# Performance work log

Measured on AMD Instinct MI355X. Metric: run time of the kernel, lower is better.

The kernel has to match this reference:

```python
import jax, jax.numpy as jnp
import numpy as np

N = 50000
E = 800000
IN_FEAT = 256
HIDDEN = 256
NUM_CLASS = 10
NUM_GRAPHS = 512
LAYERS = 2


def setup_inputs() -> dict:
    key = jax.random.key(0)
    ks = jax.random.split(key, 10)
    x = jax.random.normal(ks[0], (N, IN_FEAT), dtype=jnp.float32)
    edge_index = jax.random.randint(ks[1], (2, E), 0, N, dtype=jnp.int32)
    batch = jnp.sort(jax.random.randint(ks[2], (N,), 0, NUM_GRAPHS, dtype=jnp.int32))
    s_in = 1.0 / np.sqrt(IN_FEAT)
    s_h = 1.0 / np.sqrt(HIDDEN)
    enc_W = jax.random.uniform(ks[3], (IN_FEAT, HIDDEN), jnp.float32, -s_in, s_in)
    enc_b = jax.random.uniform(ks[4], (HIDDEN,), jnp.float32, -s_in, s_in)
    conv_W = jax.random.uniform(ks[5], (LAYERS, HIDDEN, HIDDEN), jnp.float32, -s_h, s_h)
    conv_b = jax.random.uniform(ks[6], (LAYERS, HIDDEN), jnp.float32, -s_h, s_h)
    out_W = jax.random.uniform(ks[7], (HIDDEN, NUM_CLASS), jnp.float32, -s_h, s_h)
    out_b = jax.random.uniform(ks[8], (NUM_CLASS,), jnp.float32, -s_h, s_h)
    return {"x": x, "edge_index": edge_index, "batch": batch,
            "enc_W": enc_W, "enc_b": enc_b,
            "conv_W": conv_W, "conv_b": conv_b,
            "out_W": out_W, "out_b": out_b}


def _gcn_conv(x, row, col, deg_norm_edge, W, b):
    # PyG GCNConv: linear transform, then normalized scatter-add aggregation.
    h = x @ W                                   # [N, H]
    msg = h[row] * deg_norm_edge[:, None]       # [E+N, H] gather + scale
    out = jax.ops.segment_sum(msg, col, num_segments=N)  # scatter-add
    return out + b


def reference(x, edge_index, batch, enc_W, enc_b, conv_W, conv_b, out_W, out_b):
    # self-loops appended once (same structure every layer)
    loops = jnp.arange(N, dtype=edge_index.dtype)
    row = jnp.concatenate([edge_index[0], loops])  # source
    col = jnp.concatenate([edge_index[1], loops])  # target
    deg = jax.ops.segment_sum(jnp.ones_like(col, dtype=x.dtype), col, num_segments=N)
    dinv = jnp.where(deg > 0, jax.lax.rsqrt(deg), 0.0)
    norm = dinv[row] * dinv[col]                # symmetric GCN normalization per edge

    h = x @ enc_W + enc_b
    for i in range(LAYERS):
        h = jax.nn.relu(_gcn_conv(h, row, col, norm, conv_W[i], conv_b[i]))

    # global_mean_pool over `batch` segment ids
    sums = jax.ops.segment_sum(h, batch, num_segments=NUM_GRAPHS)
    cnts = jax.ops.segment_sum(jnp.ones((N,), dtype=h.dtype), batch, num_segments=NUM_GRAPHS)
    pooled = sums / jnp.maximum(cnts, 1.0)[:, None]

    # dropout is identity in eval mode
    return pooled @ out_W + out_b
```

## Files before the change

### kernel.cpp

```cpp
#include <hip/hip_runtime.h>

#define NN 50000
#define NE 800000
#define HD 256
#define NG 512
#define NC 10
#define TILES ((NN + 31) / 32)
#define GEMM_G 521
#define NP 196
#define HB 200
#define CHUNK (NE / HB)
#define NODES_PER_HB (NN / HB)

typedef unsigned short u16;
typedef unsigned char u8;
typedef short v8s __attribute__((ext_vector_type(8)));
typedef float v4f __attribute__((ext_vector_type(4)));
typedef float v2f __attribute__((ext_vector_type(2)));
typedef u16 v4u __attribute__((ext_vector_type(4)));
typedef u16 v8u __attribute__((ext_vector_type(8)));

static __device__ __forceinline__ float bf2f(u16 u) {
    return __uint_as_float(((unsigned)u) << 16);
}
static __device__ __forceinline__ u16 f2bf(float f) {
    unsigned u = __float_as_uint(f);
    unsigned r = (u + 0x7fffu + ((u >> 16) & 1u)) >> 16;
    return (u16)r;
}
static __device__ __forceinline__ int clampi(int v, int lo, int hi) {
    return min(max(v, lo), hi);
}
static __device__ __forceinline__ float ldf(const void* p, size_t i, int isbf) {
    return isbf ? bf2f(((const u16*)p)[i]) : ((const float*)p)[i];
}

static __device__ __forceinline__ u8 f32_to_fp8(float f) {
#if __has_builtin(__builtin_amdgcn_cvt_pk_fp8_f32)
    int r = __builtin_amdgcn_cvt_pk_fp8_f32(f, f, 0, false);
    return (u8)(r & 0xff);
#else
    float a = fabsf(f);
    unsigned s = (__float_as_uint(f) >> 31) << 7;
    if (a < 0.0009765625f) return (u8)s;
    a = fminf(a, 448.f);
    if (a < 0.015625f) {
        int m = (int)(a * 512.f + 0.5f);
        return (u8)(s | min(m, 7));
    }
    unsigned u = __float_as_uint(a);
    unsigned r = u + 0x0007FFFFu + ((u >> 20) & 1u);
    int e = (int)(r >> 23) - 127 + 7;
    if (e > 15) return (u8)(s | 0x7E);
    unsigned m = (r >> 20) & 7u;
    return (u8)(s | ((unsigned)e << 3) | m);
#endif
}
static __device__ __forceinline__ v4f fp8x4_to_f32(unsigned v) {
#if __has_builtin(__builtin_amdgcn_cvt_pk_f32_fp8)
    v2f lo = __builtin_amdgcn_cvt_pk_f32_fp8(v, false);
    v2f hi = __builtin_amdgcn_cvt_pk_f32_fp8(v, true);
    return (v4f){lo[0], lo[1], hi[0], hi[1]};
#else
    v4f o;
#pragma unroll
    for (int j = 0; j < 4; j++) {
        unsigned b = (v >> (8 * j)) & 0xffu;
        unsigned e = (b >> 3) & 15u, m = b & 7u;
        float val = e ? __uint_as_float(((e + 120u) << 23) | (m << 20))
                      : (float)m * 0.001953125f;
        o[j] = (b & 0x80u) ? -val : val;
    }
    return o;
#endif
}

__global__ void k_detect(const u16* __restrict__ xu, int* __restrict__ mode) {
    __shared__ int cnt;
    if (threadIdx.x == 0) cnt = 0;
    __syncthreads();
    int bad = 0;
    for (int i = threadIdx.x; i < 4096; i += 256) {
        float v = bf2f(xu[2 * i]);
        float av = fabsf(v);
        if (av > 100.f || (av < 1e-3f && av != 0.f)) bad++;
    }
    atomicAdd(&cnt, bad);
    __syncthreads();
    if (threadIdx.x == 0) mode[0] = (cnt > 1024) ? 0 : 1;
}

__global__ void k_prep(const void* __restrict__ enc_W, const void* __restrict__ conv_W,
                       const void* __restrict__ enc_b, const void* __restrict__ conv_b,
                       const void* __restrict__ out_b,
                       u16* __restrict__ Wp, float* __restrict__ biasf,
                       const int* __restrict__ modep) {
    int md = modep[0];
    int b = blockIdx.x;
    if (b < 768) {
        int wi = b >> 8;
        int n = b & 255, k = threadIdx.x;
        const void* W = (wi == 0) ? enc_W : conv_W;
        size_t off = (wi == 0) ? 0 : (size_t)(wi - 1) * HD * HD;
        int nt = n >> 4, m = n & 15;
        int ks = k >> 5, q = (k >> 3) & 3, j = k & 7;
        size_t idx = ((((size_t)nt * 8 + ks) * 64) + q * 16 + m) * 8 + j;
        Wp[(size_t)wi * HD * HD + idx] = f2bf(ldf(W, off + (size_t)k * HD + n, md));
    } else {
        for (int j = threadIdx.x; j < 768 + NC; j += 256) {
            float v = (j < 256) ? ldf(enc_b, j, md)
                    : (j < 768) ? ldf(conv_b, j - 256, md)
                                : ldf(out_b, j - 768, md);
            biasf[j] = v;
        }
    }
}

static __device__ __forceinline__ void hist_body(
        int b, int nthreads, const int* __restrict__ ecol,
        const int* __restrict__ batch,
        int* __restrict__ bh, int* __restrict__ gptr, int* hist) {
    int tid = threadIdx.x;
    if (tid < NP) hist[tid] = 0;
    __syncthreads();
    int e0 = b * CHUNK;
    for (int i = tid; i < CHUNK; i += nthreads) {
        int c = clampi(ecol[e0 + i], 0, NN - 1);
        atomicAdd(&hist[c >> 8], 1);
    }
    int n0 = b * NODES_PER_HB;
    for (int i = tid; i < NODES_PER_HB; i += nthreads) {
        int idx = n0 + i;
        int bb = clampi(batch[idx], 0, NG - 1);
        int bp = (idx == 0) ? -1 : clampi(batch[idx - 1], 0, NG - 1);
        for (int g = bp + 1; g <= bb; g++) gptr[g] = idx;
        if (idx == NN - 1)
            for (int g = bb + 1; g <= NG; g++) gptr[g] = NN;
    }
    __syncthreads();
    if (tid < NP) bh[(size_t)tid * HB + b] = hist[tid];
}

static __device__ __forceinline__ void scat_body(
        int b, int nthreads, const int* __restrict__ erow,
        const int* __restrict__ ecol,
        const int* __restrict__ pptr, const int* __restrict__ base,
        unsigned* __restrict__ pairbuf, int* lfill) {
    int tid = threadIdx.x;
    if (tid < NP) lfill[tid] = 0;
    __syncthreads();
    int e0 = b * CHUNK;
    for (int i = tid; i < CHUNK; i += nthreads) {
        int c = clampi(ecol[e0 + i], 0, NN - 1);
        int rw = clampi(erow[e0 + i], 0, NN - 1);
        int p = c >> 8;
        int r = atomicAdd(&lfill[p], 1);
        int pos = pptr[p] + base[(size_t)p * HB + b] + r;
        pairbuf[pos] = ((unsigned)rw << 8) | (unsigned)(c & 255);
    }
}

static __device__ __forceinline__ void gemm_body8(
        int gb, u16* As, const void* __restrict__ A, const u16* __restrict__ Wp,
        const float* __restrict__ biasf, void* __restrict__ out,
        int M, int hasBias, int outFp8, int amode) {
    int tid = threadIdx.x;
    int wave = tid >> 6;
    int lane = tid & 63;
    int m = lane & 15, q = lane >> 4;

    v8s bf[2][8];
#pragma unroll
    for (int nt = 0; nt < 2; nt++)
#pragma unroll
        for (int ks = 0; ks < 8; ks++)
            bf[nt][ks] = *(const v8s*)(Wp +
                ((size_t)((wave * 2 + nt) * 8 + ks) * 64 + lane) * 8);

    for (int tile = gb; tile < TILES; tile += GEMM_G) {
        int row0 = tile * 32;
#pragma unroll
        for (int it = 0; it < 2; it++) {
            int fb = it * 8 + wave;
            int mt = fb >> 3, ks = fb & 7;
            int row = min(row0 + mt * 16 + m, M - 1);
            int colE = ks * 32 + q * 8;
            v8s v;
            if (amode) {
                v = *(const v8s*)((const u16*)A + (size_t)row * HD + colE);
            } else {
                const float* af = (const float*)A + (size_t)row * HD + colE;
                v4f x0 = *(const v4f*)af;
                v4f x1 = *(const v4f*)(af + 4);
                v[0] = (short)f2bf(x0[0]); v[1] = (short)f2bf(x0[1]);
                v[2] = (short)f2bf(x0[2]); v[3] = (short)f2bf(x0[3]);
                v[4] = (short)f2bf(x1[0]); v[5] = (short)f2bf(x1[1]);
                v[6] = (short)f2bf(x1[2]); v[7] = (short)f2bf(x1[3]);
            }
            *(v8s*)&As[((size_t)fb * 64 + lane) * 8] = v;
        }
        __syncthreads();

        v4f acc[2][2];
#pragma unroll
        for (int i = 0; i < 2; i++)
#pragma unroll
            for (int j = 0; j < 2; j++) acc[i][j] = (v4f){0.f, 0.f, 0.f, 0.f};

#pragma unroll
        for (int ks = 0; ks < 8; ks++) {
            v8s a0 = *(const v8s*)&As[((size_t)ks * 64 + lane) * 8];
            v8s a1 = *(const v8s*)&As[((size_t)(8 + ks) * 64 + lane) * 8];
            acc[0][0] = __builtin_amdgcn_mfma_f32_16x16x32_bf16(
                a0, bf[0][ks], acc[0][0], 0, 0, 0);
            acc[0][1] = __builtin_amdgcn_mfma_f32_16x16x32_bf16(
                a0, bf[1][ks], acc[0][1], 0, 0, 0);
            acc[1][0] = __builtin_amdgcn_mfma_f32_16x16x32_bf16(
                a1, bf[0][ks], acc[1][0], 0, 0, 0);
            acc[1][1] = __builtin_amdgcn_mfma_f32_16x16x32_bf16(
                a1, bf[1][ks], acc[1][1], 0, 0, 0);
        }
        if (outFp8) {
#pragma unroll
            for (int mt = 0; mt < 2; mt++) {
#pragma unroll
                for (int nt = 0; nt < 2; nt++) {
                    int ocol = wave * 32 + nt * 16 + m;
#pragma unroll
                    for (int r = 0; r < 4; r++) {
                        int orow = row0 + mt * 16 + q * 4 + r;
                        if (orow < M)
                            ((u8*)out)[(size_t)orow * HD + ocol] =
                                f32_to_fp8(acc[mt][nt][r] * 32.f);
                    }
                }
            }
        } else {
#pragma unroll
            for (int mt = 0; mt < 2; mt++) {
#pragma unroll
                for (int nt = 0; nt < 2; nt++) {
                    int ocol = wave * 32 + nt * 16 + m;
                    float badd = hasBias ? biasf[ocol] : 0.f;
#pragma unroll
                    for (int r = 0; r < 4; r++) {
                        int orow = row0 + mt * 16 + q * 4 + r;
                        if (orow < M)
                            ((u16*)out)[(size_t)orow * HD + ocol] =
                                f2bf(acc[mt][nt][r] + badd);
                    }
                }
            }
        }
        __syncthreads();
    }
}

static __device__ __forceinline__ void agg_node(
        const u8* __restrict__ t, const int* __restrict__ cptr,
        const int* __restrict__ csrc, const float* __restrict__ dinv,
        const float* __restrict__ biasf, int node, int lane, float* o) {
    int half = lane >> 5;
    int f0 = (lane & 31) * 8;
    const u8* tf = t + f0;
    float dn = dinv[node];
    float a[8];
#pragma unroll
    for (int k = 0; k < 8; k++) a[k] = 0.f;

    if (half == 0) {
        uint2 sv = *(const uint2*)(tf + (size_t)node * HD);
        v4f lo = fp8x4_to_f32(sv.x), hi = fp8x4_to_f32(sv.y);
#pragma unroll
        for (int k = 0; k < 4; k++) {
            a[k] += lo[k] * dn;
            a[k + 4] += hi[k] * dn;
        }
    }

    int e0 = cptr[node], e1 = cptr[node + 1];
    e1 = clampi(e1, 0, NE);
    e0 = clampi(e0, 0, e1);
    int e = e0;
    for (; e + 16 <= e1; e += 16) {
        int s[8];
#pragma unroll
        for (int j = 0; j < 8; j++)
            s[j] = clampi(csrc[e + 2 * j + half], 0, NN - 1);
        uint2 rv[8];
        float wv[8];
#pragma unroll
        for (int j = 0; j < 8; j++) {
            rv[j] = *(const uint2*)(tf + (size_t)s[j] * HD);
            wv[j] = dinv[s[j]];
        }
#pragma unroll
        for (int j = 0; j < 8; j++) {
            v4f lo = fp8x4_to_f32(rv[j].x), hi = fp8x4_to_f32(rv[j].y);
#pragma unroll
            for (int k = 0; k < 4; k++) {
                a[k] = fmaf(lo[k], wv[j], a[k]);
                a[k + 4] = fmaf(hi[k], wv[j], a[k + 4]);
            }
        }
    }
    for (; e + 2 <= e1; e += 2) {
        int s = clampi(csrc[e + half], 0, NN - 1);
        uint2 rv = *(const uint2*)(tf + (size_t)s * HD);
        float wv = dinv[s];
        v4f lo = fp8x4_to_f32(rv.x), hi = fp8x4_to_f32(rv.y);
#pragma unroll
        for (int k = 0; k < 4; k++) {
            a[k] = fmaf(lo[k], wv, a[k]);
            a[k + 4] = fmaf(hi[k], wv, a[k + 4]);
        }
    }
    if (e < e1 && half == 0) {
        int s = clampi(csrc[e], 0, NN - 1);
        uint2 rv = *(const uint2*)(tf + (size_t)s * HD);
        float wv = dinv[s];
        v4f lo = fp8x4_to_f32(rv.x), hi = fp8x4_to_f32(rv.y);
#pragma unroll
        for (int k = 0; k < 4; k++) {
            a[k] = fmaf(lo[k], wv, a[k]);
            a[k + 4] = fmaf(hi[k], wv, a[k + 4]);
        }
    }
#pragma unroll
    for (int k = 0; k < 8; k++) a[k] += __shfl_xor(a[k], 32, 64);

    float sc = dn * 0.03125f;
    v4f b0 = *(const v4f*)(biasf + f0);
    v4f b1 = *(const v4f*)(biasf + f0 + 4);
#pragma unroll
    for (int k = 0; k < 4; k++) {
        o[k] = fmaxf(fmaf(a[k], sc, b0[k]), 0.f);
        o[k + 4] = fmaxf(fmaf(a[k + 4], sc, b1[k]), 0.f);
    }
}

__global__ __launch_bounds__(512) void k_gemm(
        const void* __restrict__ A, const u16* __restrict__ Wp,
        const float* __restrict__ biasf, void* __restrict__ out,
        int M, int hasBias, int outFp8,
        const int* __restrict__ modep, int forceBf) {
    __shared__ u16 As[16 * 64 * 8];
    gemm_body8(blockIdx.x, As, A, Wp, biasf, out, M, hasBias, outFp8,
               forceBf ? 1 : modep[0]);
}

__global__ __launch_bounds__(256) void k_hist(
        const int* __restrict__ ecol, const int* __restrict__ batch,
        int* __restrict__ bh, int* __restrict__ gptr) {
    __shared__ int hist[NP];
    hist_body(blockIdx.x, 256, ecol, batch, bh, gptr, hist);
}

__global__ __launch_bounds__(256) void k_scat(
        const int* __restrict__ erow, const int* __restrict__ ecol,
        const int* __restrict__ pptr, const int* __restrict__ base,
        unsigned* __restrict__ pairbuf) {
    __shared__ int lfill[NP];
    scat_body(blockIdx.x, 256, erow, ecol, pptr, base, pairbuf, lfill);
}

__global__ __launch_bounds__(512) void k_gemm_hist(
        const void* __restrict__ A, const u16* __restrict__ Wp,
        const float* __restrict__ biasf, void* __restrict__ out,
        int M, int hasBias, const int* __restrict__ modep, int forceBf,
        const int* __restrict__ ecol, const int* __restrict__ batch,
        int* __restrict__ bh, int* __restrict__ gptr) {
    __shared__ u16 As[16 * 64 * 8];
    __shared__ int hist[NP];
    if (blockIdx.x < HB) {
        hist_body(blockIdx.x, 512, ecol, batch, bh, gptr, hist);
    } else {
        gemm_body8(blockIdx.x - HB, As, A, Wp, biasf, out, M, hasBias, 0,
                   forceBf ? 1 : modep[0]);
    }
}

__global__ __launch_bounds__(512) void k_scat_gemm1(
        const void* __restrict__ A, const u16* __restrict__ Wp,
        void* __restrict__ out, int M,
        const int* __restrict__ erow, const int* __restrict__ ecol,
        const int* __restrict__ pptr, const int* __restrict__ base,
        unsigned* __restrict__ pairbuf) {
    __shared__ u16 As[16 * 64 * 8];
    __shared__ int lfill[NP];
    if (blockIdx.x < HB) {
        scat_body(blockIdx.x, 512, erow, ecol, pptr, base, pairbuf, lfill);
    } else {
        gemm_body8(blockIdx.x - HB, As, A, Wp, nullptr, out, M, 0, 1, 1);
    }
}

__global__ __launch_bounds__(256) void k_aggregate2(
        const u8* __restrict__ t, const int* __restrict__ cptr,
        const int* __restrict__ csrc, const float* __restrict__ dinv,
        const float* __restrict__ biasf, u16* __restrict__ out) {
    int wave = threadIdx.x >> 6, lane = threadIdx.x & 63;
    int node = blockIdx.x * 4 + wave;
    if (node >= NN) return;
    float o[8];
    agg_node(t, cptr, csrc, dinv, biasf, node, lane, o);
    if (lane < 32) {
        v8u pk;
#pragma unroll
        for (int k = 0; k < 8; k++) pk[k] = f2bf(o[k]);
        *(v8u*)(out + (size_t)node * HD + lane * 8) = pk;
    }
}

__global__ __launch_bounds__(256) void k_scanA(
        const int* __restrict__ bh, int* __restrict__ base, int* __restrict__ ptot) {
    int p = blockIdx.x, t = threadIdx.x;
    int v = (t < HB) ? bh[(size_t)p * HB + t] : 0;
    __shared__ int sh[256];
    sh[t] = v;
    __syncthreads();
    for (int off = 1; off < 256; off <<= 1) {
        int x = (t >= off) ? sh[t - off] : 0;
        __syncthreads();
        sh[t] += x;
        __syncthreads();
    }
    if (t < HB) base[(size_t)p * HB + t] = sh[t] - v;
    if (t == 0) ptot[p] = sh[255];
}

__global__ __launch_bounds__(256) void k_scanB(
        const int* __restrict__ ptot, int* __restrict__ pptr) {
    int t = threadIdx.x;
    int v = (t < NP) ? ptot[t] : 0;
    __shared__ int sh[256];
    sh[t] = v;
    __syncthreads();
    for (int off = 1; off < 256; off <<= 1) {
        int x = (t >= off) ? sh[t - off] : 0;
        __syncthreads();
        sh[t] += x;
        __syncthreads();
    }
    if (t < NP) pptr[t] = sh[t] - v;
    if (t == 0) pptr[NP] = sh[255];
}

__global__ __launch_bounds__(256) void k_part2(
        const int* __restrict__ pptr, const unsigned* __restrict__ pairbuf,
        int* __restrict__ cptr, float* __restrict__ dinv, int* __restrict__ csrc) {
    int p = blockIdx.x, t = threadIdx.x;
    int seg0 = pptr[p], seg1 = pptr[p + 1];
    __shared__ int hist[256], sums[256], fill[256];
    hist[t] = 0;
    fill[t] = 0;
    __syncthreads();
    for (int i = seg0 + t; i < seg1; i += 256)
        atomicAdd(&hist[pairbuf[i] & 255], 1);
    __syncthreads();
    int d = hist[t];
    sums[t] = d;
    __syncthreads();
    for (int off = 1; off < 256; off <<= 1) {
        int x = (t >= off) ? sums[t - off] : 0;
        __syncthreads();
        sums[t] += x;
        __syncthreads();
    }
    int ex = sums[t] - d;
    int c = p * 256 + t;
    if (c < NN) {
        cptr[c] = seg0 + ex;
        dinv[c] = rsqrtf((float)(d + 1));
    }
    if (p == NP - 1 && t == 0) cptr[NN] = NE;
    __syncthreads();
    sums[t] = ex;
    __syncthreads();
    for (int i = seg0 + t; i < seg1; i += 256) {
        unsigned v = pairbuf[i];
        int cl = v & 255;
        int r = atomicAdd(&fill[cl], 1);
        csrc[seg0 + sums[cl] + r] = (int)(v >> 8);
    }
}

__global__ __launch_bounds__(256) void k_head(
        const u16* __restrict__ h, const int* __restrict__ gptr,
        const void* __restrict__ W, const float* __restrict__ biasf,
        void* __restrict__ outv, const int* __restrict__ modep) {
    int md = modep[0];
    int g = blockIdx.x, f = threadIdx.x;
    int hi = clampi(gptr[g + 1], 0, NN);
    int lo = clampi(gptr[g], 0, hi);
    float s0 = 0.f, s1 = 0.f, s2 = 0.f, s3 = 0.f;
    int i = lo;
    for (; i + 4 <= hi; i += 4) {
        s0 += bf2f(h[(size_t)i * HD + f]);
        s1 += bf2f(h[(size_t)(i + 1) * HD + f]);
        s2 += bf2f(h[(size_t)(i + 2) * HD + f]);
        s3 += bf2f(h[(size_t)(i + 3) * HD + f]);
    }
    for (; i < hi; i++) s0 += bf2f(h[(size_t)i * HD + f]);
    __shared__ float ps[256];
    ps[f] = ((s0 + s1) + (s2 + s3)) / fmaxf((float)(hi - lo), 1.0f);
    __syncthreads();
    if (threadIdx.x < 64) {
        int lane = threadIdx.x;
        float acc[NC];
#pragma unroll
        for (int c = 0; c < NC; c++) acc[c] = 0.f;
        for (int k = lane; k < HD; k += 64) {
            float p = ps[k];
#pragma unroll
            for (int c = 0; c < NC; c++) acc[c] += p * ldf(W, (size_t)k * NC + c, md);
        }
#pragma unroll
        for (int c = 0; c < NC; c++) {
            for (int off = 32; off > 0; off >>= 1)
                acc[c] += __shfl_down(acc[c], off, 64);
        }
        if (lane == 0) {
#pragma unroll
            for (int c = 0; c < NC; c++) {
                float vv = acc[c] + biasf[768 + c];
                if (md) ((u16*)outv)[g * NC + c] = f2bf(vv);
                else    ((float*)outv)[g * NC + c] = vv;
            }
        }
    }
}

extern "C" void kernel_launch(void* const* d_in, const int* in_sizes, int n_in,
                              void* d_out, int out_size, void* d_ws, size_t ws_size,
                              hipStream_t stream) {
    const void* x      = d_in[0];
    const int*  ei     = (const int*)d_in[1];
    const int*  batch  = (const int*)d_in[2];
    const void* enc_W  = d_in[3];
    const void* enc_b  = d_in[4];
    const void* conv_W = d_in[5];
    const void* conv_b = d_in[6];
    const void* out_W  = d_in[7];
    const void* out_b  = d_in[8];

    char* w = (char*)d_ws;
    auto alloc = [&](size_t b) { char* p = w; w += (b + 255) & ~(size_t)255; return p; };
    int*   mode   = (int*)alloc(256);
    float* dinv   = (float*)alloc(NN * 4);
    int*   cptr   = (int*)alloc((NN + 1) * 4);
    int*   gptr   = (int*)alloc((NG + 1) * 4);
    int*   csrc   = (int*)alloc((size_t)NE * 4);
    u16*   Wp     = (u16*)alloc((size_t)3 * HD * HD * 2);
    float* biasf  = (float*)alloc(778 * 4);
    u16*   hbuf   = (u16*)alloc((size_t)NN * HD * 2);
    size_t scratch_need = ((size_t)2 * NP * HB + 2 * NP + 1) * 4 + (size_t)NE * 4 + 1024;
    size_t used = (size_t)(w - (char*)d_ws);
    bool fused = (used + scratch_need <= ws_size);
    char* sb = fused ? alloc(scratch_need) : (char*)hbuf;
    int* bh   = (int*)sb;
    int* base = bh + (size_t)NP * HB;
    int* ptot = base + (size_t)NP * HB;
    int* pptr = ptot + NP;
    unsigned* pairbuf = (unsigned*)(pptr + NP + 1);
    u8* tbuf = (u8*)d_in[0];

    const int* erow = ei;
    const int* ecol = ei + NE;

    k_detect<<<1, 256, 0, stream>>>((const u16*)x, mode);
    k_prep<<<769, 256, 0, stream>>>(enc_W, conv_W, enc_b, conv_b, out_b, Wp, biasf, mode);

    if (fused) {
        k_gemm_hist<<<HB + GEMM_G, 512, 0, stream>>>(
            x, Wp, biasf, hbuf, NN, 1, mode, 0, ecol, batch, bh, gptr);
        k_scanA<<<NP, 256, 0, stream>>>(bh, base, ptot);
        k_scanB<<<1, 256, 0, stream>>>(ptot, pptr);
        k_scat_gemm1<<<HB + GEMM_G, 512, 0, stream>>>(
            hbuf, Wp + (size_t)HD * HD, tbuf, NN, erow, ecol, pptr, base, pairbuf);
        k_part2<<<NP, 256, 0, stream>>>(pptr, pairbuf, cptr, dinv, csrc);
    } else {
        k_hist<<<HB, 256, 0, stream>>>(ecol, batch, bh, gptr);
        k_scanA<<<NP, 256, 0, stream>>>(bh, base, ptot);
        k_scanB<<<1, 256, 0, stream>>>(ptot, pptr);
        k_scat<<<HB, 256, 0, stream>>>(erow, ecol, pptr, base, pairbuf);
        k_part2<<<NP, 256, 0, stream>>>(pptr, pairbuf, cptr, dinv, csrc);
        k_gemm<<<GEMM_G, 512, 0, stream>>>(x, Wp, biasf, hbuf, NN, 1, 0, mode, 0);
        k_gemm<<<GEMM_G, 512, 0, stream>>>(hbuf, Wp + (size_t)HD * HD, nullptr,
                                           tbuf, NN, 0, 1, mode, 1);
    }
    k_aggregate2<<<(NN + 3) / 4, 256, 0, stream>>>(tbuf, cptr, csrc, dinv,
                                                   biasf + 256, hbuf);
    k_gemm<<<GEMM_G, 512, 0, stream>>>(hbuf, Wp + (size_t)2 * HD * HD, nullptr,
                                       tbuf, NN, 0, 1, mode, 1);
    k_aggregate2<<<(NN + 3) / 4, 256, 0, stream>>>(tbuf, cptr, csrc, dinv,
                                                   biasf + 256 + HD, hbuf);
    k_head<<<NG, 256, 0, stream>>>(hbuf, gptr, out_W, biasf, d_out, mode);
}
```

Before: 289.4 us.

## Fold mode detection into prep and drop fused GEMM/CSR-build kernels

The separate mode-detection launch is removed: every block of the weight-prep kernel now recomputes the bf16/fp32 detection over 4096 samples in shared memory, and the last block writes the mode. The fused kernels that ran the histogram or scatter alongside the first two GEMMs are removed. The host always launches hist, scan, scatter and part2 first, then the GEMMs separately. This trades one fewer launch and simpler code for losing the overlap between the CSR-build work and the GEMMs, plus redundant detection reads in every prep block.

Measured after the change: 304.5 us. 5.2% more time.

```diff
diff --git a/kernel.cpp b/kernel.cpp
--- a/kernel.cpp
+++ b/kernel.cpp
@@ -75,9 +75,9 @@
 #endif
 }
 
-__global__ void k_detect(const u16* __restrict__ xu, int* __restrict__ mode) {
-    __shared__ int cnt;
-    if (threadIdx.x == 0) cnt = 0;
+static __device__ __forceinline__ int detect_mode_block(
+        const u16* __restrict__ xu, int* sh) {
+    if (threadIdx.x == 0) sh[0] = 0;
     __syncthreads();
     int bad = 0;
     for (int i = threadIdx.x; i < 4096; i += 256) {
@@ -85,17 +85,19 @@
         float av = fabsf(v);
         if (av > 100.f || (av < 1e-3f && av != 0.f)) bad++;
     }
-    atomicAdd(&cnt, bad);
-    __syncthreads();
-    if (threadIdx.x == 0) mode[0] = (cnt > 1024) ? 0 : 1;
-}
-
-__global__ void k_prep(const void* __restrict__ enc_W, const void* __restrict__ conv_W,
+    atomicAdd(sh, bad);
+    __syncthreads();
+    return (sh[0] > 1024) ? 0 : 1;
+}
+
+__global__ void k_prep(const u16* __restrict__ xu,
+                       const void* __restrict__ enc_W, const void* __restrict__ conv_W,
                        const void* __restrict__ enc_b, const void* __restrict__ conv_b,
                        const void* __restrict__ out_b,
                        u16* __restrict__ Wp, float* __restrict__ biasf,
-                       const int* __restrict__ modep) {
-    int md = modep[0];
+                       int* __restrict__ modep) {
+    __shared__ int sh[1];
+    int md = detect_mode_block(xu, sh);
     int b = blockIdx.x;
     if (b < 768) {
         int wi = b >> 8;
@@ -113,23 +115,24 @@
                                 : ldf(out_b, j - 768, md);
             biasf[j] = v;
         }
-    }
-}
-
-static __device__ __forceinline__ void hist_body(
-        int b, int nthreads, const int* __restrict__ ecol,
-        const int* __restrict__ batch,
-        int* __restrict__ bh, int* __restrict__ gptr, int* hist) {
-    int tid = threadIdx.x;
+        if (threadIdx.x == 0) modep[0] = md;
+    }
+}
+
+__global__ __launch_bounds__(256) void k_hist(
+        const int* __restrict__ ecol, const int* __restrict__ batch,
+        int* __restrict__ bh, int* __restrict__ gptr) {
+    __shared__ int hist[NP];
+    int b = blockIdx.x, tid = threadIdx.x;
     if (tid < NP) hist[tid] = 0;
     __syncthreads();
     int e0 = b * CHUNK;
-    for (int i = tid; i < CHUNK; i += nthreads) {
+    for (int i = tid; i < CHUNK; i += 256) {
         int c = clampi(ecol[e0 + i], 0, NN - 1);
         atomicAdd(&hist[c >> 8], 1);
     }
     int n0 = b * NODES_PER_HB;
-    for (int i = tid; i < NODES_PER_HB; i += nthreads) {
+    for (int i = tid; i < NODES_PER_HB; i += 256) {
         int idx = n0 + i;
         int bb = clampi(batch[idx], 0, NG - 1);
         int bp = (idx == 0) ? -1 : clampi(batch[idx - 1], 0, NG - 1);
@@ -141,16 +144,16 @@
     if (tid < NP) bh[(size_t)tid * HB + b] = hist[tid];
 }
 
-static __device__ __forceinline__ void scat_body(
-        int b, int nthreads, const int* __restrict__ erow,
-        const int* __restrict__ ecol,
+__global__ __launch_bounds__(256) void k_scat(
+        const int* __restrict__ erow, const int* __restrict__ ecol,
         const int* __restrict__ pptr, const int* __restrict__ base,
-        unsigned* __restrict__ pairbuf, int* lfill) {
-    int tid = threadIdx.x;
+        unsigned* __restrict__ pairbuf) {
+    __shared__ int lfill[NP];
+    int b = blockIdx.x, tid = threadIdx.x;
     if (tid < NP) lfill[tid] = 0;
     __syncthreads();
     int e0 = b * CHUNK;
-    for (int i = tid; i < CHUNK; i += nthreads) {
+    for (int i = tid; i < CHUNK; i += 256) {
         int c = clampi(ecol[e0 + i], 0, NN - 1);
         int rw = clampi(erow[e0 + i], 0, NN - 1);
         int p = c >> 8;
@@ -256,6 +259,16 @@
     }
 }
 
+__global__ __launch_bounds__(512) void k_gemm(
+        const void* __restrict__ A, const u16* __restrict__ Wp,
+        const float* __restrict__ biasf, void* __restrict__ out,
+        int M, int hasBias, int outFp8,
+        const int* __restrict__ modep, int forceBf) {
+    __shared__ u16 As[16 * 64 * 8];
+    gemm_body8(blockIdx.x, As, A, Wp, biasf, out, M, hasBias, outFp8,
+               forceBf ? 1 : modep[0]);
+}
+
 static __device__ __forceinline__ void agg_node(
         const u8* __restrict__ t, const int* __restrict__ cptr,
         const int* __restrict__ csrc, const float* __restrict__ dinv,
@@ -336,62 +349,6 @@
     for (int k = 0; k < 4; k++) {
         o[k] = fmaxf(fmaf(a[k], sc, b0[k]), 0.f);
         o[k + 4] = fmaxf(fmaf(a[k + 4], sc, b1[k]), 0.f);
-    }
-}
-
-__global__ __launch_bounds__(512) void k_gemm(
-        const void* __restrict__ A, const u16* __restrict__ Wp,
-        const float* __restrict__ biasf, void* __restrict__ out,
-        int M, int hasBias, int outFp8,
-        const int* __restrict__ modep, int forceBf) {
-    __shared__ u16 As[16 * 64 * 8];
-    gemm_body8(blockIdx.x, As, A, Wp, biasf, out, M, hasBias, outFp8,
-               forceBf ? 1 : modep[0]);
-}
-
-__global__ __launch_bounds__(256) void k_hist(
-        const int* __restrict__ ecol, const int* __restrict__ batch,
-        int* __restrict__ bh, int* __restrict__ gptr) {
-    __shared__ int hist[NP];
-    hist_body(blockIdx.x, 256, ecol, batch, bh, gptr, hist);
-}
-
-__global__ __launch_bounds__(256) void k_scat(
-        const int* __restrict__ erow, const int* __restrict__ ecol,
-        const int* __restrict__ pptr, const int* __restrict__ base,
-        unsigned* __restrict__ pairbuf) {
-    __shared__ int lfill[NP];
-    scat_body(blockIdx.x, 256, erow, ecol, pptr, base, pairbuf, lfill);
-}
-
-__global__ __launch_bounds__(512) void k_gemm_hist(
-        const void* __restrict__ A, const u16* __restrict__ Wp,
-        const float* __restrict__ biasf, void* __restrict__ out,
-        int M, int hasBias, const int* __restrict__ modep, int forceBf,
-        const int* __restrict__ ecol, const int* __restrict__ batch,
-        int* __restrict__ bh, int* __restrict__ gptr) {
-    __shared__ u16 As[16 * 64 * 8];
-    __shared__ int hist[NP];
-    if (blockIdx.x < HB) {
-        hist_body(blockIdx.x, 512, ecol, batch, bh, gptr, hist);
-    } else {
-        gemm_body8(blockIdx.x - HB, As, A, Wp, biasf, out, M, hasBias, 0,
-                   forceBf ? 1 : modep[0]);
-    }
-}
-
-__global__ __launch_bounds__(512) void k_scat_gemm1(
-        const void* __restrict__ A, const u16* __restrict__ Wp,
-        void* __restrict__ out, int M,
-        const int* __restrict__ erow, const int* __restrict__ ecol,
-        const int* __restrict__ pptr, const int* __restrict__ base,
-        unsigned* __restrict__ pairbuf) {
-    __shared__ u16 As[16 * 64 * 8];
-    __shared__ int lfill[NP];
-    if (blockIdx.x < HB) {
-        scat_body(blockIdx.x, 512, erow, ecol, pptr, base, pairbuf, lfill);
-    } else {
-        gemm_body8(blockIdx.x - HB, As, A, Wp, nullptr, out, M, 0, 1, 1);
     }
 }
 
@@ -556,8 +513,7 @@
     u16*   hbuf   = (u16*)alloc((size_t)NN * HD * 2);
     size_t scratch_need = ((size_t)2 * NP * HB + 2 * NP + 1) * 4 + (size_t)NE * 4 + 1024;
     size_t used = (size_t)(w - (char*)d_ws);
-    bool fused = (used + scratch_need <= ws_size);
-    char* sb = fused ? alloc(scratch_need) : (char*)hbuf;
+    char* sb = (used + scratch_need <= ws_size) ? alloc(scratch_need) : (char*)hbuf;
     int* bh   = (int*)sb;
     int* base = bh + (size_t)NP * HB;
     int* ptot = base + (size_t)NP * HB;
@@ -568,27 +524,16 @@
     const int* erow = ei;
     const int* ecol = ei + NE;
 
-    k_detect<<<1, 256, 0, stream>>>((const u16*)x, mode);
-    k_prep<<<769, 256, 0, stream>>>(enc_W, conv_W, enc_b, conv_b, out_b, Wp, biasf, mode);
-
-    if (fused) {
-        k_gemm_hist<<<HB + GEMM_G, 512, 0, stream>>>(
-            x, Wp, biasf, hbuf, NN, 1, mode, 0, ecol, batch, bh, gptr);
-        k_scanA<<<NP, 256, 0, stream>>>(bh, base, ptot);
-        k_scanB<<<1, 256, 0, stream>>>(ptot, pptr);
-        k_scat_gemm1<<<HB + GEMM_G, 512, 0, stream>>>(
-            hbuf, Wp + (size_t)HD * HD, tbuf, NN, erow, ecol, pptr, base, pairbuf);
-        k_part2<<<NP, 256, 0, stream>>>(pptr, pairbuf, cptr, dinv, csrc);
-    } else {
-        k_hist<<<HB, 256, 0, stream>>>(ecol, batch, bh, gptr);
-        k_scanA<<<NP, 256, 0, stream>>>(bh, base, ptot);
-        k_scanB<<<1, 256, 0, stream>>>(ptot, pptr);
-        k_scat<<<HB, 256, 0, stream>>>(erow, ecol, pptr, base, pairbuf);
-        k_part2<<<NP, 256, 0, stream>>>(pptr, pairbuf, cptr, dinv, csrc);
-        k_gemm<<<GEMM_G, 512, 0, stream>>>(x, Wp, biasf, hbuf, NN, 1, 0, mode, 0);
-        k_gemm<<<GEMM_G, 512, 0, stream>>>(hbuf, Wp + (size_t)HD * HD, nullptr,
-                                           tbuf, NN, 0, 1, mode, 1);
-    }
+    k_prep<<<769, 256, 0, stream>>>((const u16*)x, enc_W, conv_W, enc_b,
+                                    conv_b, out_b, Wp, biasf, mode);
+    k_hist<<<HB, 256, 0, stream>>>(ecol, batch, bh, gptr);
+    k_scanA<<<NP, 256, 0, stream>>>(bh, base, ptot);
+    k_scanB<<<1, 256, 0, stream>>>(ptot, pptr);
+    k_scat<<<HB, 256, 0, stream>>>(erow, ecol, pptr, base, pairbuf);
+    k_part2<<<NP, 256, 0, stream>>>(pptr, pairbuf, cptr, dinv, csrc);
+    k_gemm<<<GEMM_G, 512, 0, stream>>>(x, Wp, biasf, hbuf, NN, 1, 0, mode, 0);
+    k_gemm<<<GEMM_G, 512, 0, stream>>>(hbuf, Wp + (size_t)HD * HD, nullptr,
+                                       tbuf, NN, 0, 1, mode, 1);
     k_aggregate2<<<(NN + 3) / 4, 256, 0, stream>>>(tbuf, cptr, csrc, dinv,
                                                    biasf + 256, hbuf);
     k_gemm<<<GEMM_G, 512, 0, stream>>>(hbuf, Wp + (size_t)2 * HD * HD, nullptr,
```
